# Kernel tuning notes

Measured on AMD Instinct MI355X. Metric: run time of the kernel, lower is better.

Reference implementation:

```python
import jax, jax.numpy as jnp
import numpy as np

NUM_CLASSES = 10
LABEL_SMOOTHING = 0.1
GAMMA = 2.0
TRANSFORM_PENALTY = 0.2
EXACT_MATCH_BONUS = 5.0
CREATIVITY_WEIGHT = 0.15


def setup_inputs() -> dict:
    key = jax.random.key(0)
    k1, k2, k3, k4 = jax.random.split(key, 4)
    B, C, H, W = 512, NUM_CLASSES, 64, 64
    return {
        "pred_output": jax.random.normal(k1, (B, C, H, W), dtype=jnp.float32),
        "targets": jax.random.randint(k2, (B, H, W), 0, NUM_CLASSES, dtype=jnp.int32),
        "inputs": jax.random.randint(k3, (B, H, W), 0, NUM_CLASSES, dtype=jnp.int32),
        "strategic_reasoning": jax.random.normal(k4, (B, 128), dtype=jnp.float32),
    }


def _diversity_bonus(pred_idx):
    # Encode each 2x2 window as a base-10 integer (colors in [0,10) -> code < 10000),
    # then count distinct codes per sample with a presence bitmap (GPU-friendly dedup).
    B, H, W = pred_idx.shape
    codes = (pred_idx[:, :-1, :-1] * 1000 + pred_idx[:, :-1, 1:] * 100
             + pred_idx[:, 1:, :-1] * 10 + pred_idx[:, 1:, 1:])  # [B, H-1, W-1]
    codes = codes.reshape(B, -1)

    def count_unique(c):
        present = jnp.zeros((NUM_CLASSES ** 4,), dtype=jnp.float32).at[c].set(1.0)
        return present.sum()

    n_unique = jax.vmap(count_unique)(codes)  # [B]
    diversity = n_unique / ((H - 1) * (W - 1))
    return diversity.mean() * 0.02


def reference(pred_output, targets, inputs, strategic_reasoning):
    B, C, H, W = pred_output.shape

    # Label smoothing (applied to the one-hot targets; argmax is unchanged,
    # matching the original where CE is taken on the argmax'ed indices).
    targets_oh = jax.nn.one_hot(targets, C, axis=1, dtype=pred_output.dtype)
    smooth_targets = targets_oh * (1.0 - LABEL_SMOOTHING) + LABEL_SMOOTHING / C
    target_idx = jnp.argmax(smooth_targets, axis=1)  # == targets

    # Strategic focal loss
    logp = jax.nn.log_softmax(pred_output, axis=1)  # [B,C,H,W]
    ce = -jnp.take_along_axis(logp, target_idx[:, None, :, :], axis=1)[:, 0]  # [B,H,W]
    pt = jnp.exp(-ce)
    present = jax.nn.one_hot(targets, C, dtype=jnp.float32).max(axis=(1, 2))  # [B,C]
    unique_colors = present.sum(axis=-1)  # [B]
    strategic_weights = jnp.where(unique_colors > 3, 1.2, 1.0)  # [B]
    focal_loss = ((1.0 - pt) ** GAMMA * ce * strategic_weights[:, None, None]).mean()

    # Exact match / IoU stats
    pred_idx = jnp.argmax(pred_output, axis=1)  # [B,H,W]
    eq = (pred_idx == target_idx)
    exact_matches_strict = jnp.all(eq, axis=(1, 2)).astype(jnp.float32)
    intersection = eq.astype(jnp.float32).sum(axis=(1, 2))
    union = H * W
    iou_scores = intersection / union
    combined_matches = 0.2 * exact_matches_strict + 0.8 * iou_scores
    exact_count = combined_matches.sum()
    exact_bonus = jnp.maximum(-combined_matches.mean() * EXACT_MATCH_BONUS, -3.0)

    # Copy penalty
    copy_penalty = jnp.all(pred_idx == inputs, axis=(1, 2)).astype(jnp.float32)
    transform_penalty = copy_penalty.mean() * TRANSFORM_PENALTY

    # Creativity bonus
    creativity_bonus = jax.nn.sigmoid(strategic_reasoning).mean() * CREATIVITY_WEIGHT

    # Pattern diversity bonus
    diversity_bonus = _diversity_bonus(pred_idx)

    # Grid complexity bonus (H > 15 for our shapes)
    grid_size_factor = jnp.minimum(H * W / 900.0, 1.0)
    grid_complexity_bonus = combined_matches.mean() * grid_size_factor * 0.05

    total_loss = (focal_loss + transform_penalty + exact_bonus
                  - creativity_bonus - diversity_bonus - grid_complexity_bonus)
    bad = jnp.isnan(total_loss) | jnp.isinf(total_loss)
    total_loss = jnp.where(bad, jnp.minimum(focal_loss, 10.0), total_loss)

    return (total_loss, focal_loss, transform_penalty, exact_bonus, exact_count,
            combined_matches.sum(), iou_scores.mean(), creativity_bonus,
            diversity_bonus, grid_complexity_bonus)
```

## Files before the change

kernel.cpp:

```cpp
#include <hip/hip_runtime.h>
#include <math.h>

#define B_    512
#define C_    10
#define HW_   4096
#define NTA   1024
#define NTF   512
#define NBMP  313

__device__ __forceinline__ float wave_sum_f(float v) {
#pragma unroll
    for (int off = 32; off > 0; off >>= 1) v += __shfl_xor(v, off, 64);
    return v;
}

__global__ __launch_bounds__(NTA, 8) void loss_main(
    const float* __restrict__ pred, const int* __restrict__ tgt,
    const int* __restrict__ inp, const float* __restrict__ strat,
    float* __restrict__ ws)
{
    const int b   = blockIdx.x;
    const int tid = threadIdx.x;

    __shared__ unsigned int s_pred32[HW_ / 4];
    __shared__ unsigned int s_bmp[NBMP];
    __shared__ float        s_red[16][5];
    __shared__ unsigned int s_cmask;

    if (tid < NBMP) s_bmp[tid] = 0u;
    if (tid == 0) s_cmask = 0u;

    const int p = tid << 2;
    const float* pb = pred + (size_t)b * (C_ * HW_) + p;
    const int4 t4 = *(const int4*)(tgt + b * HW_ + p);

    float focal = 0.f;
    unsigned pack = 0u, cmask = 0u;
    int eqc = 0;

#pragma unroll
    for (int h = 0; h < 2; ++h) {
        float x[C_][2];
#pragma unroll
        for (int c = 0; c < C_; ++c) {
            const float2 v = *(const float2*)(pb + c * HW_ + h * 2);
            x[c][0] = v.x; x[c][1] = v.y;
        }
#pragma unroll
        for (int e2 = 0; e2 < 2; ++e2) {
            const int e = h * 2 + e2;
            const int t = (e == 0) ? t4.x : (e == 1) ? t4.y : (e == 2) ? t4.z : t4.w;
            cmask |= 1u << t;
            float mx = x[0][e2]; int am = 0;
#pragma unroll
            for (int c = 1; c < C_; ++c)
                if (x[c][e2] > mx) { mx = x[c][e2]; am = c; }
            float se = 0.f, xt = 0.f;
#pragma unroll
            for (int c = 0; c < C_; ++c) {
                se += __expf(x[c][e2] - mx);
                if (c == t) xt = x[c][e2];
            }
            const float ce = (mx + __logf(se)) - xt;
            const float pt = __expf(-ce);
            const float om = 1.f - pt;
            focal += om * om * ce;
            eqc += (am == t);
            pack |= (unsigned)am << (8 * e);
        }
    }
    s_pred32[tid] = pack;

    const int4 i4 = *(const int4*)(inp + b * HW_ + p);
    const int dfc = ((int)((pack      ) & 0xffu) != i4.x)
                  + ((int)((pack >>  8) & 0xffu) != i4.y)
                  + ((int)((pack >> 16) & 0xffu) != i4.z)
                  + ((int)((pack >> 24) & 0xffu) != i4.w);

    float cre = 0.f;
    if (tid < 128) {
        const float sv = strat[b * 128 + tid];
        cre = 1.f / (1.f + __expf(-sv));
    }

    __syncthreads();

    {
        const int r  = tid >> 4;
        const int c4 = (tid & 15) << 2;
        if (r < 63) {
            const int di = tid;
            const unsigned w0 = s_pred32[di];
            const unsigned w1 = s_pred32[di + 16];
            const unsigned n0 = (c4 < 60) ? s_pred32[di + 1]  : 0u;
            const unsigned n1 = (c4 < 60) ? s_pred32[di + 17] : 0u;
            const unsigned a0 =  w0        & 0xffu, a1 = (w0 >>  8) & 0xffu,
                           a2 = (w0 >> 16) & 0xffu, a3 = (w0 >> 24) & 0xffu,
                           a4 =  n0        & 0xffu;
            const unsigned b0 =  w1        & 0xffu, b1 = (w1 >>  8) & 0xffu,
                           b2 = (w1 >> 16) & 0xffu, b3 = (w1 >> 24) & 0xffu,
                           b4 =  n1        & 0xffu;
            unsigned code;
            code = a0 * 1000u + a1 * 100u + b0 * 10u + b1;
            atomicOr(&s_bmp[code >> 5], 1u << (code & 31u));
            code = a1 * 1000u + a2 * 100u + b1 * 10u + b2;
            atomicOr(&s_bmp[code >> 5], 1u << (code & 31u));
            code = a2 * 1000u + a3 * 100u + b2 * 10u + b3;
            atomicOr(&s_bmp[code >> 5], 1u << (code & 31u));
            if (c4 < 60) {
                code = a3 * 1000u + a4 * 100u + b3 * 10u + b4;
                atomicOr(&s_bmp[code >> 5], 1u << (code & 31u));
            }
        }
    }
    __syncthreads();

    const int nu = (tid < NBMP) ? __popc(s_bmp[tid]) : 0;

    const float rf = wave_sum_f(focal);
    const float re = wave_sum_f((float)eqc);
    const float rd = wave_sum_f((float)dfc);
    const float rc = wave_sum_f(cre);
    const float rn = wave_sum_f((float)nu);
#pragma unroll
    for (int off = 32; off > 0; off >>= 1)
        cmask |= (unsigned)__shfl_xor((int)cmask, off, 64);

    const int wv = tid >> 6;
    if ((tid & 63) == 0) {
        s_red[wv][0] = rf; s_red[wv][1] = re; s_red[wv][2] = rd;
        s_red[wv][3] = rc; s_red[wv][4] = rn;
        atomicOr(&s_cmask, cmask);
    }
    __syncthreads();
    if (tid == 0) {
        float F = 0.f, E = 0.f, D = 0.f, CR = 0.f, NU = 0.f;
#pragma unroll
        for (int i = 0; i < 16; ++i) {
            F += s_red[i][0]; E += s_red[i][1]; D += s_red[i][2];
            CR += s_red[i][3]; NU += s_red[i][4];
        }
        const int uc = __popc(s_cmask);
        const float sw = (uc > 3) ? 1.2f : 1.0f;
        ws[0 * B_ + b] = F * sw;
        ws[1 * B_ + b] = E;
        ws[2 * B_ + b] = (E == 4096.f) ? 1.f : 0.f;
        ws[3 * B_ + b] = (D == 0.f) ? 1.f : 0.f;
        ws[4 * B_ + b] = NU;
        ws[5 * B_ + b] = CR;
    }
}

__device__ __forceinline__ float block_sum(float v, volatile float* sp, int tid) {
#pragma unroll
    for (int off = 32; off > 0; off >>= 1) v += __shfl_down(v, off, 64);
    __syncthreads();
    if ((tid & 63) == 0) sp[tid >> 6] = v;
    __syncthreads();
    float s = 0.f;
    if (tid == 0) {
#pragma unroll
        for (int i = 0; i < NTF / 64; ++i) s += sp[i];
    }
    return s;
}

__global__ __launch_bounds__(NTF) void loss_final(
    const float* __restrict__ ws, float* __restrict__ out)
{
    const int tid = threadIdx.x;
    __shared__ float s_red[NTF / 64];

    const float focal_b = ws[0 * B_ + tid];
    const float inter   = ws[1 * B_ + tid];
    const float strict  = ws[2 * B_ + tid];
    const float copyf   = ws[3 * B_ + tid];
    const float nu      = ws[4 * B_ + tid];
    const float cre     = ws[5 * B_ + tid];

    const float iou  = inter * (1.f / 4096.f);
    const float comb = 0.2f * strict + 0.8f * iou;
    const float divb = nu * (1.f / 3969.f);

    const float focal_s = block_sum(focal_b, s_red, tid);
    const float comb_s  = block_sum(comb, s_red, tid);
    const float iou_s   = block_sum(iou, s_red, tid);
    const float copy_s  = block_sum(copyf, s_red, tid);
    const float div_s   = block_sum(divb, s_red, tid);
    const float cre_s   = block_sum(cre, s_red, tid);

    if (tid == 0) {
        const float focal_loss        = focal_s / (512.f * 4096.f);
        const float comb_mean         = comb_s / 512.f;
        const float exact_count       = comb_s;
        const float exact_bonus       = fmaxf(-comb_mean * 5.f, -3.f);
        const float transform_penalty = (copy_s / 512.f) * 0.2f;
        const float creativity        = (cre_s / (512.f * 128.f)) * 0.15f;
        const float diversity         = (div_s / 512.f) * 0.02f;
        const float gcb               = comb_mean * 0.05f;

        float total = focal_loss + transform_penalty + exact_bonus
                    - creativity - diversity - gcb;
        if (isnan(total) || isinf(total)) total = fminf(focal_loss, 10.f);

        out[0] = total;
        out[1] = focal_loss;
        out[2] = transform_penalty;
        out[3] = exact_bonus;
        out[4] = exact_count;
        out[5] = exact_count;
        out[6] = iou_s / 512.f;
        out[7] = creativity;
        out[8] = diversity;
        out[9] = gcb;
    }
}

extern "C" void kernel_launch(void* const* d_in, const int* in_sizes, int n_in,
                              void* d_out, int out_size, void* d_ws, size_t ws_size,
                              hipStream_t stream)
{
    const float* pred  = (const float*)d_in[0];
    const int*   tgt   = (const int*)d_in[1];
    const int*   inp   = (const int*)d_in[2];
    const float* strat = (const float*)d_in[3];
    float* ws  = (float*)d_ws;
    float* out = (float*)d_out;

    hipLaunchKernelGGL(loss_main, dim3(B_), dim3(NTA), 0, stream,
                       pred, tgt, inp, strat, ws);
    hipLaunchKernelGGL(loss_final, dim3(1), dim3(NTF), 0, stream, ws, out);
}
```

Measured before the change: 33.41 us.

## Fuse final reduction into main kernel via last-block ticket, widen per-thread loads

The two-kernel structure is merged into one. The last block to finish, identified by an atomic ticket counter, performs the cross-sample reduction and writes the outputs. Each block now uses 512 threads, and each thread handles 8 pixels using float4 nontemporal loads, so the global loads are wider and the final kernel launch disappears. In exchange it adds a memset launch for the ticket, plus threadfence and atomic overhead, and it lowers the thread count per block.

```diff
diff --git a/kernel.cpp b/kernel.cpp
--- a/kernel.cpp
+++ b/kernel.cpp
@@ -4,78 +4,100 @@
 #define B_    512
 #define C_    10
 #define HW_   4096
-#define NTA   1024
-#define NTF   512
+#define NT    512
 #define NBMP  313
 
+typedef float f4v __attribute__((ext_vector_type(4)));
+typedef int   i4v __attribute__((ext_vector_type(4)));
+
+__device__ __forceinline__ f4v ntld_f4(const float* p) {
+    return __builtin_nontemporal_load((const f4v*)p);
+}
+__device__ __forceinline__ i4v ntld_i4(const int* p) {
+    return __builtin_nontemporal_load((const i4v*)p);
+}
 __device__ __forceinline__ float wave_sum_f(float v) {
 #pragma unroll
     for (int off = 32; off > 0; off >>= 1) v += __shfl_xor(v, off, 64);
     return v;
 }
-
-__global__ __launch_bounds__(NTA, 8) void loss_main(
+__device__ __forceinline__ float block_sum(float v, volatile float* sp, int tid) {
+    v = wave_sum_f(v);
+    __syncthreads();
+    if ((tid & 63) == 0) sp[tid >> 6] = v;
+    __syncthreads();
+    float s = 0.f;
+    if (tid == 0) {
+#pragma unroll
+        for (int i = 0; i < NT / 64; ++i) s += sp[i];
+    }
+    return s;
+}
+__device__ __forceinline__ float agld(const float* p) {
+    return __hip_atomic_load(p, __ATOMIC_RELAXED, __HIP_MEMORY_SCOPE_AGENT);
+}
+
+__global__ __launch_bounds__(NT, 4) void loss_all(
     const float* __restrict__ pred, const int* __restrict__ tgt,
     const int* __restrict__ inp, const float* __restrict__ strat,
-    float* __restrict__ ws)
+    float* __restrict__ ws, float* __restrict__ out,
+    unsigned int* __restrict__ ticket)
 {
     const int b   = blockIdx.x;
     const int tid = threadIdx.x;
 
     __shared__ unsigned int s_pred32[HW_ / 4];
     __shared__ unsigned int s_bmp[NBMP];
-    __shared__ float        s_red[16][5];
+    __shared__ float        s_red[8][5];
     __shared__ unsigned int s_cmask;
+    __shared__ int          s_last;
 
     if (tid < NBMP) s_bmp[tid] = 0u;
     if (tid == 0) s_cmask = 0u;
 
-    const int p = tid << 2;
-    const float* pb = pred + (size_t)b * (C_ * HW_) + p;
-    const int4 t4 = *(const int4*)(tgt + b * HW_ + p);
+    const float* pb = pred + (size_t)b * (C_ * HW_);
 
     float focal = 0.f;
-    unsigned pack = 0u, cmask = 0u;
-    int eqc = 0;
-
-#pragma unroll
-    for (int h = 0; h < 2; ++h) {
-        float x[C_][2];
+    unsigned cmask = 0u;
+    int eqc = 0, dfc = 0;
+
+#pragma unroll
+    for (int k = 0; k < 2; ++k) {
+        const int p = (k * NT + tid) * 4;
+        const i4v t4 = ntld_i4(tgt + b * HW_ + p);
+        const i4v i4 = ntld_i4(inp + b * HW_ + p);
+        float x[C_][4];
 #pragma unroll
         for (int c = 0; c < C_; ++c) {
-            const float2 v = *(const float2*)(pb + c * HW_ + h * 2);
-            x[c][0] = v.x; x[c][1] = v.y;
-        }
-#pragma unroll
-        for (int e2 = 0; e2 < 2; ++e2) {
-            const int e = h * 2 + e2;
-            const int t = (e == 0) ? t4.x : (e == 1) ? t4.y : (e == 2) ? t4.z : t4.w;
+            const f4v v = ntld_f4(pb + c * HW_ + p);
+            x[c][0] = v.x; x[c][1] = v.y; x[c][2] = v.z; x[c][3] = v.w;
+        }
+        unsigned pack = 0u;
+#pragma unroll
+        for (int e = 0; e < 4; ++e) {
+            const int t  = (e == 0) ? t4.x : (e == 1) ? t4.y : (e == 2) ? t4.z : t4.w;
+            const int iv = (e == 0) ? i4.x : (e == 1) ? i4.y : (e == 2) ? i4.z : i4.w;
             cmask |= 1u << t;
-            float mx = x[0][e2]; int am = 0;
+            float mx = x[0][e]; int am = 0;
 #pragma unroll
             for (int c = 1; c < C_; ++c)
-                if (x[c][e2] > mx) { mx = x[c][e2]; am = c; }
+                if (x[c][e] > mx) { mx = x[c][e]; am = c; }
             float se = 0.f, xt = 0.f;
 #pragma unroll
             for (int c = 0; c < C_; ++c) {
-                se += __expf(x[c][e2] - mx);
-                if (c == t) xt = x[c][e2];
+                se += __expf(x[c][e] - mx);
+                if (c == t) xt = x[c][e];
             }
             const float ce = (mx + __logf(se)) - xt;
             const float pt = __expf(-ce);
             const float om = 1.f - pt;
             focal += om * om * ce;
             eqc += (am == t);
+            dfc += (am != iv);
             pack |= (unsigned)am << (8 * e);
         }
-    }
-    s_pred32[tid] = pack;
-
-    const int4 i4 = *(const int4*)(inp + b * HW_ + p);
-    const int dfc = ((int)((pack      ) & 0xffu) != i4.x)
-                  + ((int)((pack >>  8) & 0xffu) != i4.y)
-                  + ((int)((pack >> 16) & 0xffu) != i4.z)
-                  + ((int)((pack >> 24) & 0xffu) != i4.w);
+        s_pred32[k * NT + tid] = pack;
+    }
 
     float cre = 0.f;
     if (tid < 128) {
@@ -85,32 +107,28 @@
 
     __syncthreads();
 
-    {
-        const int r  = tid >> 4;
-        const int c4 = (tid & 15) << 2;
-        if (r < 63) {
-            const int di = tid;
-            const unsigned w0 = s_pred32[di];
-            const unsigned w1 = s_pred32[di + 16];
-            const unsigned n0 = (c4 < 60) ? s_pred32[di + 1]  : 0u;
-            const unsigned n1 = (c4 < 60) ? s_pred32[di + 17] : 0u;
-            const unsigned a0 =  w0        & 0xffu, a1 = (w0 >>  8) & 0xffu,
-                           a2 = (w0 >> 16) & 0xffu, a3 = (w0 >> 24) & 0xffu,
-                           a4 =  n0        & 0xffu;
-            const unsigned b0 =  w1        & 0xffu, b1 = (w1 >>  8) & 0xffu,
-                           b2 = (w1 >> 16) & 0xffu, b3 = (w1 >> 24) & 0xffu,
-                           b4 =  n1        & 0xffu;
-            unsigned code;
-            code = a0 * 1000u + a1 * 100u + b0 * 10u + b1;
+    for (int idx = tid; idx < 1008; idx += NT) {
+        const int c4 = (idx & 15) << 2;
+        const unsigned w0 = s_pred32[idx];
+        const unsigned w1 = s_pred32[idx + 16];
+        const unsigned n0 = (c4 < 60) ? s_pred32[idx + 1]  : 0u;
+        const unsigned n1 = (c4 < 60) ? s_pred32[idx + 17] : 0u;
+        const unsigned a0 =  w0        & 0xffu, a1 = (w0 >>  8) & 0xffu,
+                       a2 = (w0 >> 16) & 0xffu, a3 = (w0 >> 24) & 0xffu,
+                       a4 =  n0        & 0xffu;
+        const unsigned b0 =  w1        & 0xffu, b1 = (w1 >>  8) & 0xffu,
+                       b2 = (w1 >> 16) & 0xffu, b3 = (w1 >> 24) & 0xffu,
+                       b4 =  n1        & 0xffu;
+        unsigned code;
+        code = a0 * 1000u + a1 * 100u + b0 * 10u + b1;
+        atomicOr(&s_bmp[code >> 5], 1u << (code & 31u));
+        code = a1 * 1000u + a2 * 100u + b1 * 10u + b2;
+        atomicOr(&s_bmp[code >> 5], 1u << (code & 31u));
+        code = a2 * 1000u + a3 * 100u + b2 * 10u + b3;
+        atomicOr(&s_bmp[code >> 5], 1u << (code & 31u));
+        if (c4 < 60) {
+            code = a3 * 1000u + a4 * 100u + b3 * 10u + b4;
             atomicOr(&s_bmp[code >> 5], 1u << (code & 31u));
-            code = a1 * 1000u + a2 * 100u + b1 * 10u + b2;
-            atomicOr(&s_bmp[code >> 5], 1u << (code & 31u));
-            code = a2 * 1000u + a3 * 100u + b2 * 10u + b3;
-            atomicOr(&s_bmp[code >> 5], 1u << (code & 31u));
-            if (c4 < 60) {
-                code = a3 * 1000u + a4 * 100u + b3 * 10u + b4;
-                atomicOr(&s_bmp[code >> 5], 1u << (code & 31u));
-            }
         }
     }
     __syncthreads();
@@ -136,7 +154,7 @@
     if (tid == 0) {
         float F = 0.f, E = 0.f, D = 0.f, CR = 0.f, NU = 0.f;
 #pragma unroll
-        for (int i = 0; i < 16; ++i) {
+        for (int i = 0; i < 8; ++i) {
             F += s_red[i][0]; E += s_red[i][1]; D += s_red[i][2];
             CR += s_red[i][3]; NU += s_red[i][4];
         }
@@ -148,46 +166,33 @@
         ws[3 * B_ + b] = (D == 0.f) ? 1.f : 0.f;
         ws[4 * B_ + b] = NU;
         ws[5 * B_ + b] = CR;
-    }
-}
-
-__device__ __forceinline__ float block_sum(float v, volatile float* sp, int tid) {
-#pragma unroll
-    for (int off = 32; off > 0; off >>= 1) v += __shfl_down(v, off, 64);
-    __syncthreads();
-    if ((tid & 63) == 0) sp[tid >> 6] = v;
-    __syncthreads();
-    float s = 0.f;
-    if (tid == 0) {
-#pragma unroll
-        for (int i = 0; i < NTF / 64; ++i) s += sp[i];
-    }
-    return s;
-}
-
-__global__ __launch_bounds__(NTF) void loss_final(
-    const float* __restrict__ ws, float* __restrict__ out)
-{
-    const int tid = threadIdx.x;
-    __shared__ float s_red[NTF / 64];
-
-    const float focal_b = ws[0 * B_ + tid];
-    const float inter   = ws[1 * B_ + tid];
-    const float strict  = ws[2 * B_ + tid];
-    const float copyf   = ws[3 * B_ + tid];
-    const float nu      = ws[4 * B_ + tid];
-    const float cre     = ws[5 * B_ + tid];
+        __threadfence();
+        const unsigned old = atomicAdd(ticket, 1u);
+        s_last = (old == (unsigned)(gridDim.x - 1));
+    }
+    __syncthreads();
+    if (!s_last) return;
+
+    __threadfence();
+
+    const float focal_b = agld(ws + 0 * B_ + tid);
+    const float inter   = agld(ws + 1 * B_ + tid);
+    const float strict  = agld(ws + 2 * B_ + tid);
+    const float copyf   = agld(ws + 3 * B_ + tid);
+    const float nuv     = agld(ws + 4 * B_ + tid);
+    const float crev    = agld(ws + 5 * B_ + tid);
 
     const float iou  = inter * (1.f / 4096.f);
     const float comb = 0.2f * strict + 0.8f * iou;
-    const float divb = nu * (1.f / 3969.f);
-
-    const float focal_s = block_sum(focal_b, s_red, tid);
-    const float comb_s  = block_sum(comb, s_red, tid);
-    const float iou_s   = block_sum(iou, s_red, tid);
-    const float copy_s  = block_sum(copyf, s_red, tid);
-    const float div_s   = block_sum(divb, s_red, tid);
-    const float cre_s   = block_sum(cre, s_red, tid);
+    const float divb = nuv * (1.f / 3969.f);
+
+    volatile float* sp = &s_red[0][0];
+    const float focal_s = block_sum(focal_b, sp, tid);
+    const float comb_s  = block_sum(comb, sp, tid);
+    const float iou_s   = block_sum(iou, sp, tid);
+    const float copy_s  = block_sum(copyf, sp, tid);
+    const float div_s   = block_sum(divb, sp, tid);
+    const float cre_s   = block_sum(crev, sp, tid);
 
     if (tid == 0) {
         const float focal_loss        = focal_s / (512.f * 4096.f);
@@ -226,8 +231,9 @@
     const float* strat = (const float*)d_in[3];
     float* ws  = (float*)d_ws;
     float* out = (float*)d_out;
-
-    hipLaunchKernelGGL(loss_main, dim3(B_), dim3(NTA), 0, stream,
-                       pred, tgt, inp, strat, ws);
-    hipLaunchKernelGGL(loss_final, dim3(1), dim3(NTF), 0, stream, ws, out);
-}
+    unsigned int* ticket = (unsigned int*)(ws + 6 * B_);
+
+    hipMemsetAsync(ticket, 0, sizeof(unsigned int), stream);
+    hipLaunchKernelGGL(loss_all, dim3(B_), dim3(NT), 0, stream,
+                       pred, tgt, inp, strat, ws, out, ticket);
+}
```

Result: slower. 49.25 us (+47.4%).

## Halve block size and issue all float4 loads up front per thread

Applied to the files above, without the earlier changes.

The main kernel now runs 512 threads per block, and each thread handles 8 pixels in two float4 groups. It issues all 20 float4 prediction loads plus the target, input and strategic loads before any compute, to raise memory-level parallelism and use wider loads. The bitmap insertion loop now strides to cover all 1008 rows with fewer threads. This raises register pressure (the launch bounds hint drops to 4 waves per EU), which may lower occupancy.

```diff
diff --git a/kernel.cpp b/kernel.cpp
--- a/kernel.cpp
+++ b/kernel.cpp
@@ -4,8 +4,7 @@
 #define B_    512
 #define C_    10
 #define HW_   4096
-#define NTA   1024
-#define NTF   512
+#define NT    512
 #define NBMP  313
 
 __device__ __forceinline__ float wave_sum_f(float v) {
@@ -13,8 +12,55 @@
     for (int off = 32; off > 0; off >>= 1) v += __shfl_xor(v, off, 64);
     return v;
 }
-
-__global__ __launch_bounds__(NTA, 8) void loss_main(
+__device__ __forceinline__ float block_sum(float v, volatile float* sp, int tid) {
+    v = wave_sum_f(v);
+    __syncthreads();
+    if ((tid & 63) == 0) sp[tid >> 6] = v;
+    __syncthreads();
+    float s = 0.f;
+    if (tid == 0) {
+#pragma unroll
+        for (int i = 0; i < NT / 64; ++i) s += sp[i];
+    }
+    return s;
+}
+
+#define PROC4(X, T4, I4, SLOT)                                              \
+    {                                                                       \
+        unsigned pack = 0u;                                                 \
+        _Pragma("unroll")                                                   \
+        for (int e = 0; e < 4; ++e) {                                       \
+            const int t  = (e==0)?T4.x:(e==1)?T4.y:(e==2)?T4.z:T4.w;        \
+            const int iv = (e==0)?I4.x:(e==1)?I4.y:(e==2)?I4.z:I4.w;        \
+            cmask |= 1u << t;                                               \
+            float x0 = (e==0)?X[0].x:(e==1)?X[0].y:(e==2)?X[0].z:X[0].w;    \
+            float mx = x0; int am = 0;                                      \
+            float xs[C_];                                                   \
+            xs[0] = x0;                                                     \
+            _Pragma("unroll")                                               \
+            for (int c = 1; c < C_; ++c) {                                  \
+                const float xc = (e==0)?X[c].x:(e==1)?X[c].y:(e==2)?X[c].z:X[c].w; \
+                xs[c] = xc;                                                 \
+                if (xc > mx) { mx = xc; am = c; }  \
+            }                                                               \
+            float se = 0.f, xt = 0.f;                                       \
+            _Pragma("unroll")                                               \
+            for (int c = 0; c < C_; ++c) {                                  \
+                se += __expf(xs[c] - mx);                                   \
+                if (c == t) xt = xs[c];                                     \
+            }                                                               \
+            const float ce = (mx + __logf(se)) - xt;                        \
+            const float pt = __expf(-ce);                                   \
+            const float om = 1.f - pt;                                      \
+            focal += om * om * ce;                                          \
+            eqc += (am == t);                                               \
+            dfc += (am != iv);                                              \
+            pack |= (unsigned)am << (8 * e);                                \
+        }                                                                   \
+        s_pred32[SLOT] = pack;                                              \
+    }
+
+__global__ __launch_bounds__(NT, 4) void loss_main(
     const float* __restrict__ pred, const int* __restrict__ tgt,
     const int* __restrict__ inp, const float* __restrict__ strat,
     float* __restrict__ ws)
@@ -24,93 +70,60 @@
 
     __shared__ unsigned int s_pred32[HW_ / 4];
     __shared__ unsigned int s_bmp[NBMP];
-    __shared__ float        s_red[16][5];
+    __shared__ float        s_red[8][5];
     __shared__ unsigned int s_cmask;
 
     if (tid < NBMP) s_bmp[tid] = 0u;
     if (tid == 0) s_cmask = 0u;
 
-    const int p = tid << 2;
-    const float* pb = pred + (size_t)b * (C_ * HW_) + p;
-    const int4 t4 = *(const int4*)(tgt + b * HW_ + p);
+    const float* pb = pred + (size_t)b * (C_ * HW_);
+    const int p0 = tid * 4;
+    const int p1 = (NT + tid) * 4;
+
+    float4 xa[C_], xb[C_];
+#pragma unroll
+    for (int c = 0; c < C_; ++c) xa[c] = *(const float4*)(pb + c * HW_ + p0);
+#pragma unroll
+    for (int c = 0; c < C_; ++c) xb[c] = *(const float4*)(pb + c * HW_ + p1);
+    const int4 ta = *(const int4*)(tgt + b * HW_ + p0);
+    const int4 tb4 = *(const int4*)(tgt + b * HW_ + p1);
+    const int4 ia = *(const int4*)(inp + b * HW_ + p0);
+    const int4 ib4 = *(const int4*)(inp + b * HW_ + p1);
+    const float sv = (tid < 128) ? strat[b * 128 + tid] : 0.f;
 
     float focal = 0.f;
-    unsigned pack = 0u, cmask = 0u;
-    int eqc = 0;
-
-#pragma unroll
-    for (int h = 0; h < 2; ++h) {
-        float x[C_][2];
-#pragma unroll
-        for (int c = 0; c < C_; ++c) {
-            const float2 v = *(const float2*)(pb + c * HW_ + h * 2);
-            x[c][0] = v.x; x[c][1] = v.y;
-        }
-#pragma unroll
-        for (int e2 = 0; e2 < 2; ++e2) {
-            const int e = h * 2 + e2;
-            const int t = (e == 0) ? t4.x : (e == 1) ? t4.y : (e == 2) ? t4.z : t4.w;
-            cmask |= 1u << t;
-            float mx = x[0][e2]; int am = 0;
-#pragma unroll
-            for (int c = 1; c < C_; ++c)
-                if (x[c][e2] > mx) { mx = x[c][e2]; am = c; }
-            float se = 0.f, xt = 0.f;
-#pragma unroll
-            for (int c = 0; c < C_; ++c) {
-                se += __expf(x[c][e2] - mx);
-                if (c == t) xt = x[c][e2];
-            }
-            const float ce = (mx + __logf(se)) - xt;
-            const float pt = __expf(-ce);
-            const float om = 1.f - pt;
-            focal += om * om * ce;
-            eqc += (am == t);
-            pack |= (unsigned)am << (8 * e);
-        }
-    }
-    s_pred32[tid] = pack;
-
-    const int4 i4 = *(const int4*)(inp + b * HW_ + p);
-    const int dfc = ((int)((pack      ) & 0xffu) != i4.x)
-                  + ((int)((pack >>  8) & 0xffu) != i4.y)
-                  + ((int)((pack >> 16) & 0xffu) != i4.z)
-                  + ((int)((pack >> 24) & 0xffu) != i4.w);
-
-    float cre = 0.f;
-    if (tid < 128) {
-        const float sv = strat[b * 128 + tid];
-        cre = 1.f / (1.f + __expf(-sv));
-    }
-
-    __syncthreads();
-
-    {
-        const int r  = tid >> 4;
-        const int c4 = (tid & 15) << 2;
-        if (r < 63) {
-            const int di = tid;
-            const unsigned w0 = s_pred32[di];
-            const unsigned w1 = s_pred32[di + 16];
-            const unsigned n0 = (c4 < 60) ? s_pred32[di + 1]  : 0u;
-            const unsigned n1 = (c4 < 60) ? s_pred32[di + 17] : 0u;
-            const unsigned a0 =  w0        & 0xffu, a1 = (w0 >>  8) & 0xffu,
-                           a2 = (w0 >> 16) & 0xffu, a3 = (w0 >> 24) & 0xffu,
-                           a4 =  n0        & 0xffu;
-            const unsigned b0 =  w1        & 0xffu, b1 = (w1 >>  8) & 0xffu,
-                           b2 = (w1 >> 16) & 0xffu, b3 = (w1 >> 24) & 0xffu,
-                           b4 =  n1        & 0xffu;
-            unsigned code;
-            code = a0 * 1000u + a1 * 100u + b0 * 10u + b1;
+    unsigned cmask = 0u;
+    int eqc = 0, dfc = 0;
+
+    PROC4(xa, ta, ia, tid)
+    PROC4(xb, tb4, ib4, NT + tid)
+
+    const float cre = (tid < 128) ? 1.f / (1.f + __expf(-sv)) : 0.f;
+
+    __syncthreads();
+
+    for (int idx = tid; idx < 1008; idx += NT) {
+        const int c4 = (idx & 15) << 2;
+        const unsigned w0 = s_pred32[idx];
+        const unsigned w1 = s_pred32[idx + 16];
+        const unsigned n0 = (c4 < 60) ? s_pred32[idx + 1]  : 0u;
+        const unsigned n1 = (c4 < 60) ? s_pred32[idx + 17] : 0u;
+        const unsigned a0 =  w0        & 0xffu, a1 = (w0 >>  8) & 0xffu,
+                       a2 = (w0 >> 16) & 0xffu, a3 = (w0 >> 24) & 0xffu,
+                       a4 =  n0        & 0xffu;
+        const unsigned b0 =  w1        & 0xffu, b1 = (w1 >>  8) & 0xffu,
+                       b2 = (w1 >> 16) & 0xffu, b3 = (w1 >> 24) & 0xffu,
+                       b4 =  n1        & 0xffu;
+        unsigned code;
+        code = a0 * 1000u + a1 * 100u + b0 * 10u + b1;
+        atomicOr(&s_bmp[code >> 5], 1u << (code & 31u));
+        code = a1 * 1000u + a2 * 100u + b1 * 10u + b2;
+        atomicOr(&s_bmp[code >> 5], 1u << (code & 31u));
+        code = a2 * 1000u + a3 * 100u + b2 * 10u + b3;
+        atomicOr(&s_bmp[code >> 5], 1u << (code & 31u));
+        if (c4 < 60) {
+            code = a3 * 1000u + a4 * 100u + b3 * 10u + b4;
             atomicOr(&s_bmp[code >> 5], 1u << (code & 31u));
-            code = a1 * 1000u + a2 * 100u + b1 * 10u + b2;
-            atomicOr(&s_bmp[code >> 5], 1u << (code & 31u));
-            code = a2 * 1000u + a3 * 100u + b2 * 10u + b3;
-            atomicOr(&s_bmp[code >> 5], 1u << (code & 31u));
-            if (c4 < 60) {
-                code = a3 * 1000u + a4 * 100u + b3 * 10u + b4;
-                atomicOr(&s_bmp[code >> 5], 1u << (code & 31u));
-            }
         }
     }
     __syncthreads();
@@ -136,7 +149,7 @@
     if (tid == 0) {
         float F = 0.f, E = 0.f, D = 0.f, CR = 0.f, NU = 0.f;
 #pragma unroll
-        for (int i = 0; i < 16; ++i) {
+        for (int i = 0; i < 8; ++i) {
             F += s_red[i][0]; E += s_red[i][1]; D += s_red[i][2];
             CR += s_red[i][3]; NU += s_red[i][4];
         }
@@ -151,25 +164,11 @@
     }
 }
 
-__device__ __forceinline__ float block_sum(float v, volatile float* sp, int tid) {
-#pragma unroll
-    for (int off = 32; off > 0; off >>= 1) v += __shfl_down(v, off, 64);
-    __syncthreads();
-    if ((tid & 63) == 0) sp[tid >> 6] = v;
-    __syncthreads();
-    float s = 0.f;
-    if (tid == 0) {
-#pragma unroll
-        for (int i = 0; i < NTF / 64; ++i) s += sp[i];
-    }
-    return s;
-}
-
-__global__ __launch_bounds__(NTF) void loss_final(
+__global__ __launch_bounds__(NT) void loss_final(
     const float* __restrict__ ws, float* __restrict__ out)
 {
     const int tid = threadIdx.x;
-    __shared__ float s_red[NTF / 64];
+    __shared__ float s_red[NT / 64];
 
     const float focal_b = ws[0 * B_ + tid];
     const float inter   = ws[1 * B_ + tid];
@@ -227,7 +226,7 @@
     float* ws  = (float*)d_ws;
     float* out = (float*)d_out;
 
-    hipLaunchKernelGGL(loss_main, dim3(B_), dim3(NTA), 0, stream,
+    hipLaunchKernelGGL(loss_main, dim3(B_), dim3(NT), 0, stream,
                        pred, tgt, inp, strat, ws);
-    hipLaunchKernelGGL(loss_final, dim3(1), dim3(NTF), 0, stream, ws, out);
-}
+    hipLaunchKernelGGL(loss_final, dim3(1), dim3(NT), 0, stream, ws, out);
+}
```

Measured after the change: 28.91 us. -13.5%, faster.
